# Kernel tuning notes

Measured on AMD Instinct MI355X. Metric: run time of the kernel, lower is better.

## Reference

```python
import jax, jax.numpy as jnp
import numpy as np
from jax.scipy.special import gammaln

B = 16384
MAX_Y = 4096  # targets drawn from [0, 4096), so k ranges over 0..4095 (covers y.max())
EPS = 1e-6


def setup_inputs() -> dict:
    key = jax.random.key(0)
    k1, k2, k3 = jax.random.split(key, 3)
    r = jax.random.uniform(k1, (B, 2), dtype=jnp.float32) * 20.0 + 0.1  # NB total_count
    p = jax.random.normal(k2, (B, 2), dtype=jnp.float32)
    target = jax.random.randint(k3, (B, 2), 0, MAX_Y, dtype=jnp.int64)
    return {"r": r, "p": p, "target": target}


def _nb_logpmf(k, r, p):
    # torch NegativeBinomial(total_count=r, probs=p).log_prob(k)
    # = lgamma(k+r) - lgamma(k+1) - lgamma(r) + r*log(1-p) + k*log(p)
    return (gammaln(k + r) - gammaln(k + 1.0) - gammaln(r)
            + r * jnp.log1p(-p) + k * jnp.log(p))


def _nb_cdf_bruteforce(y, r, p):
    # brute-force: materialize (B, MAX_Y) log-PMF matrix, mask k<=y, sum
    k = jnp.arange(MAX_Y, dtype=jnp.float32)  # (K,)
    logpmf = _nb_logpmf(k[None, :], r[:, None], p[:, None])  # (B, K)
    mask = k[None, :] <= y[:, None]
    return jnp.sum(jnp.exp(logpmf) * mask, axis=1)


def reference(r, p, target):
    rho = jax.nn.relu(p[:, 1]) + 1.0
    r = jnp.clip(r, 0.0001, None)
    p1 = jnp.clip(jnp.tanh(p[:, 0]), 0.0001, 0.9999)
    y1 = target[:, 0].astype(jnp.float32)
    y2 = target[:, 1].astype(jnp.float32)
    r1, r2 = r[:, 0], r[:, 1]

    logp1 = _nb_logpmf(y1, r1, p1)
    logp2 = _nb_logpmf(y2, r2, p1)  # module reuses p1 for both marginals

    u1 = jnp.clip(_nb_cdf_bruteforce(y1, r1, p1), EPS, 1.0 - EPS)
    u2 = jnp.clip(_nb_cdf_bruteforce(y2, r2, p1), EPS, 1.0 - EPS)

    theta = jnp.maximum(rho, 1.00001)
    t1 = (-jnp.log(u1)) ** theta
    t2 = (-jnp.log(u2)) ** theta
    # original computes log(exp(-(t1+t2)**(1/theta))) — kept faithful
    logc = jnp.log(jnp.exp(-((t1 + t2) ** (1.0 / theta))))

    ll = logp1 + logp2 + logc
    return -jnp.mean(ll)
```

## Files before the change

kernel.cpp:

```cpp
#include <hip/hip_runtime.h>
#include <math.h>

#define NROWS 16384

__device__ __forceinline__ float lgam(float x) {
    float p = ((x * (x + 1.f)) * ((x + 2.f) * (x + 3.f))) *
              (((x + 4.f) * (x + 5.f)) * ((x + 6.f) * (x + 7.f)));
    float z  = x + 8.f;
    float lz = __logf(z);
    float zi = __builtin_amdgcn_rcpf(z);
    float r  = (z - 0.5f) * lz - z + 0.91893853320467f
             + zi * (0.08333333333f - 0.0027777778f * (zi * zi));
    return r - __logf(p);
}

__global__ __launch_bounds__(256) void nb_rows(
    const float* __restrict__ r,
    const float* __restrict__ p,
    const int*   __restrict__ tg,
    float* __restrict__ ws,
    float* __restrict__ out)
{
    const int tid  = threadIdx.x;
    const int lane = tid & 63;
    const int sl   = lane & 31;
    const int j    = lane >> 5;
    const int row  = blockIdx.x * 4 + (tid >> 6);

    const float rr = fmaxf(r[2 * row + j], 1e-4f);
    const float p0 = p[2 * row];
    const float e2 = __expf(2.f * p0);
    const float p1 = fminf(fmaxf(1.f - 2.f * __builtin_amdgcn_rcpf(e2 + 1.f), 1e-4f), 0.9999f);
    const int   y  = tg[2 * row + j];
    const float yf = (float)y;

    const float q1   = 1.f - p1;
    const float logp = __logf(p1);
    const float base = rr * __logf(q1) - lgam(rr);

    const float qi   = __builtin_amdgcn_rcpf(q1);
    const float mode = rr * p1 * qi;
    const float sig  = __fsqrt_rn(rr * p1) * qi;
    const int   K    = (int)fminf(mode + 12.f * sig + 32.f, yf);

    const int c = (K + 32) >> 5;
    const int s = sl * c;
    float acc = 0.f;
    if (s <= K) {
        const int   cnt = min(c, K + 1 - s);
        const float sf  = (float)s;
        const float L0  = lgam(sf + rr) - lgam(sf + 1.f) + base + sf * logp;
        float pmf = __expf(L0);
        acc = pmf;
        float kf = sf + 1.f;
        float pk = p1 * (sf + rr);
        for (int m = 1; m < cnt; ++m) {
            pmf *= pk * __builtin_amdgcn_rcpf(kf);
            acc += pmf;
            pk += p1;
            kf += 1.f;
        }
    }
    acc += __shfl_xor(acc, 1);
    acc += __shfl_xor(acc, 2);
    acc += __shfl_xor(acc, 4);
    acc += __shfl_xor(acc, 8);
    acc += __shfl_xor(acc, 16);

    const float lpy = lgam(yf + rr) - lgam(yf + 1.f) + base + yf * logp;

    const float u_own  = fminf(fmaxf(acc, 1e-6f), 1.f - 1e-6f);
    const float u_oth  = __shfl_xor(u_own, 32);
    const float lp_oth = __shfl_xor(lpy, 32);

    if (lane == 0) {
        const float rho   = fmaxf(p[2 * row + 1], 0.f) + 1.f;
        const float theta = fmaxf(rho, 1.00001f);
        const float x1 = -__logf(u_own);
        const float x2 = -__logf(u_oth);
        const float t1 = __expf(theta * __logf(x1));
        const float t2 = __expf(theta * __logf(x2));
        const float logc = -__expf(__logf(t1 + t2) * __builtin_amdgcn_rcpf(theta));
        const float nll = -(lpy + lp_oth + logc);
        if (ws) ws[row] = nll;
        else    atomicAdd(out, nll * (1.f / (float)NROWS));
    }
}

__global__ __launch_bounds__(1024) void reduce_ws(
    const float* __restrict__ ws, float* __restrict__ out)
{
    __shared__ float sm[16];
    float a = 0.f;
    for (int i = threadIdx.x; i < NROWS; i += 1024) a += ws[i];
    for (int off = 32; off > 0; off >>= 1) a += __shfl_xor(a, off);
    if ((threadIdx.x & 63) == 0) sm[threadIdx.x >> 6] = a;
    __syncthreads();
    if (threadIdx.x < 16) {
        float b = sm[threadIdx.x];
        b += __shfl_xor(b, 1);
        b += __shfl_xor(b, 2);
        b += __shfl_xor(b, 4);
        b += __shfl_xor(b, 8);
        if (threadIdx.x == 0) out[0] = b * (1.f / (float)NROWS);
    }
}

extern "C" void kernel_launch(void* const* d_in, const int* in_sizes, int n_in,
                              void* d_out, int out_size, void* d_ws, size_t ws_size,
                              hipStream_t stream) {
    const float* r  = (const float*)d_in[0];
    const float* p  = (const float*)d_in[1];
    const int*   tg = (const int*)d_in[2];
    float* out = (float*)d_out;

    if (ws_size >= NROWS * sizeof(float)) {
        float* ws = (float*)d_ws;
        nb_rows<<<NROWS / 4, 256, 0, stream>>>(r, p, tg, ws, nullptr);
        reduce_ws<<<1, 1024, 0, stream>>>(ws, out);
    } else {
        hipMemsetAsync(out, 0, sizeof(float), stream);
        nb_rows<<<NROWS / 4, 256, 0, stream>>>(r, p, tg, nullptr, out);
    }
}
```

Before: 77.23 us.

## Assign one wavefront per marginal, tighten CDF truncation, fuse lgamma differences

Each 64-lane wavefront now handles a single marginal (row, j) instead of splitting 32 lanes per marginal, so there are twice as many blocks and the per-lane chunk of the CDF sum shrinks. The two marginals of a row are combined through shared memory plus a __syncthreads instead of cross-half shuffles. The truncation bound is reduced from mode+12σ+32 to mode+6σ+16, which cuts the number of summed terms. lgamma differences are merged into one function with a single log of the ratio of the shifted products, and one Stirling correction term is dropped. The reduction kernel is unrolled. The tighter truncation and the simpler lgamma approximation risk accuracy loss on heavy-tailed rows.

After: 76.14 us. About the same (-1.4%).

```diff
diff --git a/kernel.cpp b/kernel.cpp
--- a/kernel.cpp
+++ b/kernel.cpp
@@ -3,15 +3,25 @@
 
 #define NROWS 16384
 
+__device__ __forceinline__ float prod8(float x) {
+    return ((x * (x + 1.f)) * ((x + 2.f) * (x + 3.f))) *
+           (((x + 4.f) * (x + 5.f)) * ((x + 6.f) * (x + 7.f)));
+}
+
 __device__ __forceinline__ float lgam(float x) {
-    float p = ((x * (x + 1.f)) * ((x + 2.f) * (x + 3.f))) *
-              (((x + 4.f) * (x + 5.f)) * ((x + 6.f) * (x + 7.f)));
     float z  = x + 8.f;
     float lz = __logf(z);
     float zi = __builtin_amdgcn_rcpf(z);
-    float r  = (z - 0.5f) * lz - z + 0.91893853320467f
-             + zi * (0.08333333333f - 0.0027777778f * (zi * zi));
-    return r - __logf(p);
+    return (z - 0.5f) * lz - z + 0.91893853f + 0.08333333f * zi - __logf(prod8(x));
+}
+
+__device__ __forceinline__ float lgam_diff(float a, float b) {
+    float za = a + 8.f, zb = b + 8.f;
+    float la = __logf(za), lb = __logf(zb);
+    float ra = __builtin_amdgcn_rcpf(za), rb = __builtin_amdgcn_rcpf(zb);
+    return (za - 0.5f) * la - (zb - 0.5f) * lb - (a - b)
+         + 0.08333333f * (ra - rb)
+         + __logf(prod8(b) * __builtin_amdgcn_rcpf(prod8(a)));
 }
 
 __global__ __launch_bounds__(256) void nb_rows(
@@ -21,11 +31,13 @@
     float* __restrict__ ws,
     float* __restrict__ out)
 {
+    __shared__ float su[4], sv[4];
     const int tid  = threadIdx.x;
+    const int w    = tid >> 6;
     const int lane = tid & 63;
-    const int sl   = lane & 31;
-    const int j    = lane >> 5;
-    const int row  = blockIdx.x * 4 + (tid >> 6);
+    const int rm   = blockIdx.x * 4 + w;
+    const int row  = rm >> 1;
+    const int j    = rm & 1;
 
     const float rr = fmaxf(r[2 * row + j], 1e-4f);
     const float p0 = p[2 * row];
@@ -38,19 +50,17 @@
     const float logp = __logf(p1);
     const float base = rr * __logf(q1) - lgam(rr);
 
-    const float qi   = __builtin_amdgcn_rcpf(q1);
-    const float mode = rr * p1 * qi;
-    const float sig  = __fsqrt_rn(rr * p1) * qi;
-    const int   K    = (int)fminf(mode + 12.f * sig + 32.f, yf);
+    const float qi = __builtin_amdgcn_rcpf(q1);
+    const float rp = rr * p1;
+    const int   K  = (int)fminf(fmaf(6.f, __fsqrt_rn(rp) * qi, rp * qi) + 16.f, yf);
 
-    const int c = (K + 32) >> 5;
-    const int s = sl * c;
+    const int c = (K + 64) >> 6;
+    const int s = lane * c;
     float acc = 0.f;
     if (s <= K) {
         const int   cnt = min(c, K + 1 - s);
         const float sf  = (float)s;
-        const float L0  = lgam(sf + rr) - lgam(sf + 1.f) + base + sf * logp;
-        float pmf = __expf(L0);
+        float pmf = __expf(lgam_diff(sf + rr, sf + 1.f) + base + sf * logp);
         acc = pmf;
         float kf = sf + 1.f;
         float pk = p1 * (sf + rr);
@@ -61,28 +71,27 @@
             kf += 1.f;
         }
     }
-    acc += __shfl_xor(acc, 1);
-    acc += __shfl_xor(acc, 2);
-    acc += __shfl_xor(acc, 4);
-    acc += __shfl_xor(acc, 8);
-    acc += __shfl_xor(acc, 16);
+    #pragma unroll
+    for (int off = 32; off; off >>= 1) acc += __shfl_xor(acc, off);
 
-    const float lpy = lgam(yf + rr) - lgam(yf + 1.f) + base + yf * logp;
-
-    const float u_own  = fminf(fmaxf(acc, 1e-6f), 1.f - 1e-6f);
-    const float u_oth  = __shfl_xor(u_own, 32);
-    const float lp_oth = __shfl_xor(lpy, 32);
+    const float lpy = lgam_diff(yf + rr, yf + 1.f) + base + yf * logp;
 
     if (lane == 0) {
-        const float rho   = fmaxf(p[2 * row + 1], 0.f) + 1.f;
-        const float theta = fmaxf(rho, 1.00001f);
-        const float x1 = -__logf(u_own);
-        const float x2 = -__logf(u_oth);
+        su[w] = fminf(fmaxf(acc, 1e-6f), 1.f - 1e-6f);
+        sv[w] = lpy;
+    }
+    __syncthreads();
+    if (tid < 2) {
+        const int   rrow  = blockIdx.x * 2 + tid;
+        const float u1    = su[2 * tid], u2 = su[2 * tid + 1];
+        const float theta = fmaxf(fmaxf(p[2 * rrow + 1], 0.f) + 1.f, 1.00001f);
+        const float x1 = -__logf(u1);
+        const float x2 = -__logf(u2);
         const float t1 = __expf(theta * __logf(x1));
         const float t2 = __expf(theta * __logf(x2));
         const float logc = -__expf(__logf(t1 + t2) * __builtin_amdgcn_rcpf(theta));
-        const float nll = -(lpy + lp_oth + logc);
-        if (ws) ws[row] = nll;
+        const float nll  = -(sv[2 * tid] + sv[2 * tid + 1] + logc);
+        if (ws) ws[rrow] = nll;
         else    atomicAdd(out, nll * (1.f / (float)NROWS));
     }
 }
@@ -91,18 +100,28 @@
     const float* __restrict__ ws, float* __restrict__ out)
 {
     __shared__ float sm[16];
-    float a = 0.f;
-    for (int i = threadIdx.x; i < NROWS; i += 1024) a += ws[i];
-    for (int off = 32; off > 0; off >>= 1) a += __shfl_xor(a, off);
-    if ((threadIdx.x & 63) == 0) sm[threadIdx.x >> 6] = a;
+    const int t = threadIdx.x;
+    float a0 = 0.f, a1 = 0.f, a2 = 0.f, a3 = 0.f;
+    #pragma unroll
+    for (int i = 0; i < 4; ++i) {
+        const int b = t + i * 4096;
+        a0 += ws[b];
+        a1 += ws[b + 1024];
+        a2 += ws[b + 2048];
+        a3 += ws[b + 3072];
+    }
+    float a = (a0 + a1) + (a2 + a3);
+    #pragma unroll
+    for (int off = 32; off; off >>= 1) a += __shfl_xor(a, off);
+    if ((t & 63) == 0) sm[t >> 6] = a;
     __syncthreads();
-    if (threadIdx.x < 16) {
-        float b = sm[threadIdx.x];
+    if (t < 16) {
+        float b = sm[t];
         b += __shfl_xor(b, 1);
         b += __shfl_xor(b, 2);
         b += __shfl_xor(b, 4);
         b += __shfl_xor(b, 8);
-        if (threadIdx.x == 0) out[0] = b * (1.f / (float)NROWS);
+        if (t == 0) out[0] = b * (1.f / (float)NROWS);
     }
 }
 
@@ -116,10 +135,10 @@
 
     if (ws_size >= NROWS * sizeof(float)) {
         float* ws = (float*)d_ws;
-        nb_rows<<<NROWS / 4, 256, 0, stream>>>(r, p, tg, ws, nullptr);
+        nb_rows<<<2 * NROWS / 4, 256, 0, stream>>>(r, p, tg, ws, nullptr);
         reduce_ws<<<1, 1024, 0, stream>>>(ws, out);
     } else {
         hipMemsetAsync(out, 0, sizeof(float), stream);
-        nb_rows<<<NROWS / 4, 256, 0, stream>>>(r, p, tg, nullptr, out);
+        nb_rows<<<2 * NROWS / 4, 256, 0, stream>>>(r, p, tg, nullptr, out);
     }
 }
```
